# Performance work log

Hardware: AMD Instinct MI355X
Metric: run time of the kernel (lower is better)

The kernel has to match this reference:

```python
import jax, jax.numpy as jnp
import numpy as np

DIM = 1024
N_HEADS = 16


def setup_inputs() -> dict:
    key = jax.random.key(0)
    ks = jax.random.split(key, 9)
    B, S, D = 4, 2048, DIM
    inp = {
        "q": jax.random.normal(ks[0], (B, S, D), dtype=jnp.float32),
        "k": jax.random.normal(ks[1], (B, S, D), dtype=jnp.float32),
        "v": jax.random.normal(ks[2], (B, S, D), dtype=jnp.float32),
        "mask": jnp.ones((B, S), dtype=jnp.float32),
        # nn.Linear params for q, k, v projections (weight: [out,in], bias: [out])
        "wq": jax.random.normal(ks[3], (D, D), dtype=jnp.float32) / np.sqrt(D),
        "bq": jnp.zeros((D,), dtype=jnp.float32),
        "wk": jax.random.normal(ks[4], (D, D), dtype=jnp.float32) / np.sqrt(D),
        "bk": jnp.zeros((D,), dtype=jnp.float32),
        "wv": jax.random.normal(ks[5], (D, D), dtype=jnp.float32) / np.sqrt(D),
        "bv": jnp.zeros((D,), dtype=jnp.float32),
    }
    return inp


def reference(q, k, v, mask, wq, bq, wk, bk, wv, bv):
    B, Sq, D = q.shape
    Skv = k.shape[1]
    H = N_HEADS
    Dh = D // H
    # QKV projections (nn.Linear: x @ W^T + b)
    qp = q @ wq.T + bq
    kp = k @ wk.T + bk
    vp = v @ wv.T + bv
    # split heads: (B, S, H, Dh) -> (B, H, S, Dh)
    qh = qp.reshape(B, Sq, H, Dh).transpose(0, 2, 1, 3)
    kh = kp.reshape(B, Skv, H, Dh).transpose(0, 2, 1, 3)
    vh = vp.reshape(B, Skv, H, Dh).transpose(0, 2, 1, 3)
    # scores: (B, H, Sq, Skv)
    scores = jnp.einsum("bhqd,bhkd->bhqk", qh, kh) / np.sqrt(Dh).astype(np.float32)
    # additive mask (mask is (B, kv_len) -> (B, 1, 1, kv_len))
    scores = scores - 10000.0 * (1.0 - mask[:, None, None, :])
    attn = jax.nn.softmax(scores, axis=-1)
    out = jnp.einsum("bhqk,bhkd->bhqd", attn, vh)
    # merge heads: (B, Sq, D)
    out = out.transpose(0, 2, 1, 3).reshape(B, Sq, D)
    return out
```

## Files before the change

### kernel.cpp

```cpp
#include <hip/hip_runtime.h>
#include <hip/hip_bf16.h>
#include <stdint.h>

typedef __attribute__((ext_vector_type(4))) float f32x4;
typedef __attribute__((ext_vector_type(16))) float f32x16;
typedef __attribute__((ext_vector_type(8))) short bf16x8;

#define AS1 __attribute__((address_space(1)))
#define AS3 __attribute__((address_space(3)))

#if defined(__has_builtin)
#if __has_builtin(__builtin_amdgcn_exp2f)
#define EXPF(x) __builtin_amdgcn_exp2f(x)
#define UNITS 1.4426950408889634f
#endif
#endif
#ifndef EXPF
#define EXPF(x) __expf(x)
#define UNITS 1.0f
#endif

static __device__ __forceinline__ unsigned short f2bf(float f) {
  union { float f; unsigned u; } v; v.f = f;
  unsigned r = v.u + 0x7fffu + ((v.u >> 16) & 1u);
  return (unsigned short)(r >> 16);
}

static __device__ __forceinline__ unsigned pkbf(float lo, float hi) {
  __hip_bfloat162 h2 = __float22bfloat162_rn(make_float2(lo, hi));
  union { __hip_bfloat162 h; unsigned u; } c; c.h = h2; return c.u;
}

__global__ __launch_bounds__(256) void conv_all(
    const float* __restrict__ q, const float* __restrict__ k, const float* __restrict__ v,
    const float* __restrict__ wq, const float* __restrict__ wk, const float* __restrict__ wv,
    unsigned short* __restrict__ Xq, unsigned short* __restrict__ Xk, unsigned short* __restrict__ Xv,
    unsigned short* __restrict__ Wq, unsigned short* __restrict__ Wk, unsigned short* __restrict__ Wv) {
  int bid = blockIdx.x;
  const float* src; unsigned short* dst; int base;
  if (bid < 12288) {
    int t = bid >> 12;
    base = (bid & 4095) * 2048;
    if (t == 0) { src = q; dst = Xq; }
    else if (t == 1) { src = k; dst = Xk; }
    else { src = v; dst = Xv; }
  } else {
    int r = bid - 12288;
    int t = r >> 9;
    base = (r & 511) * 2048;
    if (t == 0) { src = wq; dst = Wq; }
    else if (t == 1) { src = wk; dst = Wk; }
    else { src = wv; dst = Wv; }
  }
  int i = base + threadIdx.x * 8;
  float4 x0 = *(const float4*)(src + i);
  float4 x1 = *(const float4*)(src + i + 4);
  ushort4 o0, o1;
  o0.x = f2bf(x0.x); o0.y = f2bf(x0.y); o0.z = f2bf(x0.z); o0.w = f2bf(x0.w);
  o1.x = f2bf(x1.x); o1.y = f2bf(x1.y); o1.z = f2bf(x1.z); o1.w = f2bf(x1.w);
  *(ushort4*)(dst + i) = o0;
  *(ushort4*)(dst + i + 4) = o1;
}

__global__ __launch_bounds__(256) void proj_gemm3(
    const unsigned short* __restrict__ Xq, const unsigned short* __restrict__ Xk,
    const unsigned short* __restrict__ Xv,
    const unsigned short* __restrict__ Wqp, const unsigned short* __restrict__ Wkp,
    const unsigned short* __restrict__ Wvp,
    const float* __restrict__ bq, const float* __restrict__ bk, const float* __restrict__ bv,
    unsigned short* __restrict__ Qh, unsigned short* __restrict__ Kh,
    unsigned short* __restrict__ Vt) {
  const int K = 1024, S = 2048, H = 16;
  int z = blockIdx.z;
  const unsigned short *A, *W; const float* bias; unsigned short* dst; int transpose_v;
  if (z == 0)      { A = Xq; W = Wqp; bias = bq; dst = Qh; transpose_v = 0; }
  else if (z == 1) { A = Xk; W = Wkp; bias = bk; dst = Kh; transpose_v = 0; }
  else             { A = Xv; W = Wvp; bias = bv; dst = Vt; transpose_v = 1; }

  __shared__ unsigned short As[128 * 32];
  __shared__ unsigned short Bs[128 * 32];
  const int tid = threadIdx.x;
  const int l = tid & 63;
  const int w = tid >> 6;
  const int m0 = blockIdx.x * 128, n0 = blockIdx.y * 128;
  const int wm = w >> 1, wn = w & 1;

  f32x4 acc[4][4] = {};

  const int srow = (l >> 2);
  const int skc = (l & 3) * 8;

  for (int k0 = 0; k0 < K; k0 += 32) {
#pragma unroll
    for (int i = 0; i < 2; ++i) {
      int slot = w * 2 + i;
      int row = slot * 16 + srow;
      const unsigned short* ga = A + (long)(m0 + row) * K + k0 + skc;
      const unsigned short* gb = W + (long)(n0 + row) * K + k0 + skc;
      __builtin_amdgcn_global_load_lds((const AS1 unsigned int*)ga,
                                       (AS3 unsigned int*)(As + slot * 512 + l * 8),
                                       16, 0, 0);
      __builtin_amdgcn_global_load_lds((const AS1 unsigned int*)gb,
                                       (AS3 unsigned int*)(Bs + slot * 512 + l * 8),
                                       16, 0, 0);
    }
    __syncthreads();

    bf16x8 af[4], bfr[4];
    const int kc = (l >> 4) * 8;
#pragma unroll
    for (int mi = 0; mi < 4; ++mi)
      af[mi] = *(const bf16x8*)&As[(wm * 64 + mi * 16 + (l & 15)) * 32 + kc];
#pragma unroll
    for (int ni = 0; ni < 4; ++ni)
      bfr[ni] = *(const bf16x8*)&Bs[(wn * 64 + ni * 16 + (l & 15)) * 32 + kc];
#pragma unroll
    for (int mi = 0; mi < 4; ++mi)
#pragma unroll
      for (int ni = 0; ni < 4; ++ni)
        acc[mi][ni] = __builtin_amdgcn_mfma_f32_16x16x32_bf16(af[mi], bfr[ni], acc[mi][ni], 0, 0, 0);
    __syncthreads();
  }

#pragma unroll
  for (int ni = 0; ni < 4; ++ni) {
    int col = n0 + wn * 64 + ni * 16 + (l & 15);
    float bv_ = bias[col];
    int h = col >> 6, dh = col & 63;
#pragma unroll
    for (int mi = 0; mi < 4; ++mi) {
#pragma unroll
      for (int r = 0; r < 4; ++r) {
        int m = m0 + wm * 64 + mi * 16 + (l >> 4) * 4 + r;
        int b = m >> 11, s = m & 2047;
        unsigned short obf = f2bf(acc[mi][ni][r] + bv_);
        long addr;
        if (!transpose_v)
          addr = ((long)(b * H + h) * S + s) * 64 + dh;
        else
          addr = ((long)(b * H + h) * 64 + dh) * S + s;
        dst[addr] = obf;
      }
    }
  }
}

__device__ __forceinline__ void stage_tile(const unsigned short* __restrict__ kb,
                                           const unsigned short* __restrict__ vb,
                                           char* Kb, char* Vb, int kv0, int tid) {
  int r = tid >> 3;
  int s = (tid & 7) ^ (r & 7);
  const unsigned short* gk = kb + (kv0 + r) * 64 + s * 8;
  const unsigned short* gv = vb + r * 2048 + kv0 + s * 8;
  __builtin_amdgcn_global_load_lds((const AS1 unsigned int*)gk,
                                   (AS3 unsigned int*)(Kb + tid * 16), 16, 0, 0);
  __builtin_amdgcn_global_load_lds((const AS1 unsigned int*)gv,
                                   (AS3 unsigned int*)(Vb + tid * 16), 16, 0, 0);
}

__device__ __forceinline__ void compute_tile(const char* Kb, const char* Vb,
                                             const bf16x8 (&qf)[4],
                                             const float* __restrict__ smask,
                                             int kv0, int hi, int qc,
                                             f32x16 (&acco)[2], float& m_run, float& lrow) {
  const float kSc = 0.125f * UNITS;
  const float THR = 8.0f * UNITS;
  const int kx = qc & 7;

  bf16x8 kf[2][4], vf[2][4];
#pragma unroll
  for (int ks = 0; ks < 2; ++ks)
#pragma unroll
    for (int dc = 0; dc < 4; ++dc)
      kf[ks][dc] = *(const bf16x8*)(Kb + (ks * 32 + qc) * 128 + (((dc * 2 + hi) ^ kx) * 16));
#pragma unroll
  for (int dt = 0; dt < 2; ++dt)
#pragma unroll
    for (int c2 = 0; c2 < 4; ++c2)
      vf[dt][c2] = *(const bf16x8*)(Vb + (dt * 32 + qc) * 128 + (((c2 * 2 + hi) ^ kx) * 16));

  f32x16 st0 = {}, st1 = {};
  __builtin_amdgcn_s_setprio(1);
#pragma unroll
  for (int dc = 0; dc < 4; ++dc) {
    st0 = __builtin_amdgcn_mfma_f32_32x32x16_bf16(kf[0][dc], qf[dc], st0, 0, 0, 0);
    st1 = __builtin_amdgcn_mfma_f32_32x32x16_bf16(kf[1][dc], qf[dc], st1, 0, 0, 0);
  }
  __builtin_amdgcn_s_setprio(0);

  float mf[2][16];
#pragma unroll
  for (int ks = 0; ks < 2; ++ks)
#pragma unroll
    for (int g = 0; g < 4; ++g) {
      float4 t = *(const float4*)&smask[kv0 + ks * 32 + 4 * hi + g * 8];
      mf[ks][g * 4 + 0] = t.x; mf[ks][g * 4 + 1] = t.y;
      mf[ks][g * 4 + 2] = t.z; mf[ks][g * 4 + 3] = t.w;
    }
  float p[2][16];
#pragma unroll
  for (int r = 0; r < 16; ++r) {
    p[0][r] = fmaf(st0[r], kSc, mf[0][r]);
    p[1][r] = fmaf(st1[r], kSc, mf[1][r]);
  }

  float a0 = p[0][0], a1 = p[0][1], a2 = p[0][2], a3 = p[0][3];
#pragma unroll
  for (int r = 4; r < 16; r += 4) {
    a0 = fmaxf(a0, p[0][r]); a1 = fmaxf(a1, p[0][r + 1]);
    a2 = fmaxf(a2, p[0][r + 2]); a3 = fmaxf(a3, p[0][r + 3]);
  }
#pragma unroll
  for (int r = 0; r < 16; r += 4) {
    a0 = fmaxf(a0, p[1][r]); a1 = fmaxf(a1, p[1][r + 1]);
    a2 = fmaxf(a2, p[1][r + 2]); a3 = fmaxf(a3, p[1][r + 3]);
  }
  float pm = fmaxf(fmaxf(a0, a1), fmaxf(a2, a3));
  pm = fmaxf(pm, __shfl_xor(pm, 32));

  if (!__all(pm <= m_run + THR)) {
    float mnew = fmaxf(m_run, pm);
    float scl = EXPF(m_run - mnew);
    lrow *= scl;
#pragma unroll
    for (int dt = 0; dt < 2; ++dt)
#pragma unroll
      for (int r = 0; r < 16; ++r) acco[dt][r] *= scl;
    m_run = mnew;
  }

  float s0 = 0.f, s1 = 0.f, s2 = 0.f, s3 = 0.f;
#pragma unroll
  for (int ks = 0; ks < 2; ++ks)
#pragma unroll
    for (int r = 0; r < 16; r += 4) {
      p[ks][r]     = EXPF(p[ks][r] - m_run);     s0 += p[ks][r];
      p[ks][r + 1] = EXPF(p[ks][r + 1] - m_run); s1 += p[ks][r + 1];
      p[ks][r + 2] = EXPF(p[ks][r + 2] - m_run); s2 += p[ks][r + 2];
      p[ks][r + 3] = EXPF(p[ks][r + 3] - m_run); s3 += p[ks][r + 3];
    }
  float ps = (s0 + s1) + (s2 + s3);
  ps += __shfl_xor(ps, 32);
  lrow += ps;

#pragma unroll
  for (int ks = 0; ks < 2; ++ks) {
    unsigned cp0 = pkbf(p[ks][0], p[ks][1]);
    unsigned cp1 = pkbf(p[ks][2], p[ks][3]);
    unsigned cp2 = pkbf(p[ks][4], p[ks][5]);
    unsigned cp3 = pkbf(p[ks][6], p[ks][7]);
    unsigned cp4 = pkbf(p[ks][8], p[ks][9]);
    unsigned cp5 = pkbf(p[ks][10], p[ks][11]);
    unsigned cp6 = pkbf(p[ks][12], p[ks][13]);
    unsigned cp7 = pkbf(p[ks][14], p[ks][15]);
    asm volatile("v_permlane32_swap_b32 %0, %1" : "+v"(cp0), "+v"(cp2));
    asm volatile("v_permlane32_swap_b32 %0, %1" : "+v"(cp1), "+v"(cp3));
    asm volatile("v_permlane32_swap_b32 %0, %1" : "+v"(cp4), "+v"(cp6));
    asm volatile("v_permlane32_swap_b32 %0, %1" : "+v"(cp5), "+v"(cp7));
    union { unsigned u[4]; bf16x8 v; } B0, B1;
    B0.u[0] = cp0; B0.u[1] = cp1; B0.u[2] = cp2; B0.u[3] = cp3;
    B1.u[0] = cp4; B1.u[1] = cp5; B1.u[2] = cp6; B1.u[3] = cp7;
    __builtin_amdgcn_s_setprio(1);
    acco[0] = __builtin_amdgcn_mfma_f32_32x32x16_bf16(vf[0][ks * 2 + 0], B0.v, acco[0], 0, 0, 0);
    acco[1] = __builtin_amdgcn_mfma_f32_32x32x16_bf16(vf[1][ks * 2 + 0], B0.v, acco[1], 0, 0, 0);
    acco[0] = __builtin_amdgcn_mfma_f32_32x32x16_bf16(vf[0][ks * 2 + 1], B1.v, acco[0], 0, 0, 0);
    acco[1] = __builtin_amdgcn_mfma_f32_32x32x16_bf16(vf[1][ks * 2 + 1], B1.v, acco[1], 0, 0, 0);
    __builtin_amdgcn_s_setprio(0);
  }
}

__global__ __launch_bounds__(512, 2) void attn_kernel(const unsigned short* __restrict__ qh,
                                                      const unsigned short* __restrict__ kh,
                                                      const unsigned short* __restrict__ vt,
                                                      const float* __restrict__ mask,
                                                      float* __restrict__ out) {
  const int S = 2048;
  int bid = blockIdx.x;
  int xcd = bid & 7, jj = bid >> 3;
  int bh = xcd * 8 + (jj & 7);
  int qblk = jj >> 3;
  int b = bh >> 4, h = bh & 15;
  int tid = threadIdx.x, l = tid & 63, w = tid >> 6;
  int hi = l >> 5, qc = l & 31;

  const unsigned short* qb = qh + (long)bh * S * 64;
  const unsigned short* kb = kh + (long)bh * S * 64;
  const unsigned short* vb = vt + (long)bh * 64 * S;

  __shared__ float smask[2048];
  __shared__ __align__(16) char pool[33280];
  for (int i = tid; i < S; i += 512)
    smask[i] = (-10000.0f * UNITS) * (1.0f - mask[b * S + i]);
  __syncthreads();

  const int q0 = qblk * 256 + w * 32;

  bf16x8 qf[4];
#pragma unroll
  for (int dc = 0; dc < 4; ++dc)
    qf[dc] = *(const bf16x8*)&qb[(q0 + qc) * 64 + dc * 16 + 8 * hi];

  f32x16 acco[2] = {};
  float m_run = -1e30f, lrow = 0.0f;

  stage_tile(kb, vb, pool, pool + 8192, 0, tid);
  __syncthreads();

  for (int t = 0; t < 32; ++t) {
    char* cur = pool + (t & 1) * 16384;
    if (t < 31) {
      char* nxt = pool + ((t + 1) & 1) * 16384;
      stage_tile(kb, vb, nxt, nxt + 8192, (t + 1) * 64, tid);
    }
    compute_tile(cur, cur + 8192, qf, smask, t * 64, hi, qc, acco, m_run, lrow);
    __syncthreads();
  }

  float (*olds)[16][65] = (float (*)[16][65])pool;
  float linv = 1.0f / lrow;
#pragma unroll
  for (int pass = 0; pass < 2; ++pass) {
    if ((qc >> 4) == pass) {
#pragma unroll
      for (int dt = 0; dt < 2; ++dt)
#pragma unroll
        for (int r = 0; r < 16; ++r) {
          int d = dt * 32 + (r & 3) + 8 * (r >> 2) + 4 * hi;
          olds[w][qc & 15][d] = acco[dt][r] * linv;
        }
    }
    asm volatile("s_waitcnt lgkmcnt(0)" ::: "memory");
#pragma unroll
    for (int r = 0; r < 16; ++r) {
      float val = olds[w][r][l];
      out[((long)b * 2048 + q0 + pass * 16 + r) * 1024 + h * 64 + l] = val;
    }
    asm volatile("s_waitcnt lgkmcnt(0)" ::: "memory");
  }
}

extern "C" void kernel_launch(void* const* d_in, const int* in_sizes, int n_in,
                              void* d_out, int out_size, void* d_ws, size_t ws_size,
                              hipStream_t stream) {
  const float* q  = (const float*)d_in[0];
  const float* k  = (const float*)d_in[1];
  const float* v  = (const float*)d_in[2];
  const float* mask = (const float*)d_in[3];
  const float* wq = (const float*)d_in[4];
  const float* bq = (const float*)d_in[5];
  const float* wk = (const float*)d_in[6];
  const float* bk = (const float*)d_in[7];
  const float* wv = (const float*)d_in[8];
  const float* bv = (const float*)d_in[9];
  float* out = (float*)d_out;

  char* ws = (char*)d_ws;
  unsigned short* Xq = (unsigned short*)(ws);
  unsigned short* Xk = (unsigned short*)(ws + 16777216L);
  unsigned short* Xv = (unsigned short*)(ws + 33554432L);
  unsigned short* Wq = (unsigned short*)(ws + 50331648L);
  unsigned short* Wk = (unsigned short*)(ws + 52428800L);
  unsigned short* Wv = (unsigned short*)(ws + 54525952L);
  unsigned short* Qh = (unsigned short*)(ws + 56623104L);
  unsigned short* Kh = (unsigned short*)(ws + 73400320L);
  unsigned short* Vt = (unsigned short*)(ws + 90177536L);

  conv_all<<<13824, 256, 0, stream>>>(q, k, v, wq, wk, wv, Xq, Xk, Xv, Wq, Wk, Wv);

  dim3 ggrid(64, 8, 3);
  proj_gemm3<<<ggrid, 256, 0, stream>>>(Xq, Xk, Xv, Wq, Wk, Wv, bq, bk, bv, Qh, Kh, Vt);

  attn_kernel<<<512, 512, 0, stream>>>(Qh, Kh, Vt, mask, out);
}
```

Measured before the change: 377.2 us.

## Double-buffer projection GEMM and shrink attention blocks with direct mask reads

The projection GEMM now double-buffers its LDS tiles, so the next k-slice loads while MFMAs run on the current one, and one barrier per iteration is dropped. The attention kernel goes from 512-thread blocks covering 256 queries to 256-thread blocks covering 128 queries, launching twice as many blocks at up to 4 per CU. It also stops precomputing the mask in shared memory and instead reads the mask from global memory each tile, transforming it with an FMA. This removes the LDS mask staging and the extra barrier, but each block now repeats the K/V loads for fewer queries and makes repeated global mask reads.

```diff
diff --git a/kernel.cpp b/kernel.cpp
--- a/kernel.cpp
+++ b/kernel.cpp
@@ -77,8 +77,8 @@
   else if (z == 1) { A = Xk; W = Wkp; bias = bk; dst = Kh; transpose_v = 0; }
   else             { A = Xv; W = Wvp; bias = bv; dst = Vt; transpose_v = 1; }
 
-  __shared__ unsigned short As[128 * 32];
-  __shared__ unsigned short Bs[128 * 32];
+  __shared__ unsigned short As[2][128 * 32];
+  __shared__ unsigned short Bs[2][128 * 32];
   const int tid = threadIdx.x;
   const int l = tid & 63;
   const int w = tid >> 6;
@@ -90,37 +90,48 @@
   const int srow = (l >> 2);
   const int skc = (l & 3) * 8;
 
+#define STAGE(buf, k0)                                                            \
+  {                                                                               \
+    _Pragma("unroll")                                                             \
+    for (int i = 0; i < 2; ++i) {                                                 \
+      int slot = w * 2 + i;                                                       \
+      int row = slot * 16 + srow;                                                 \
+      const unsigned short* ga = A + (long)(m0 + row) * K + (k0) + skc;           \
+      const unsigned short* gb = W + (long)(n0 + row) * K + (k0) + skc;           \
+      __builtin_amdgcn_global_load_lds((const AS1 unsigned int*)ga,               \
+                                       (AS3 unsigned int*)(As[buf] + slot * 512 + l * 8), \
+                                       16, 0, 0);                                 \
+      __builtin_amdgcn_global_load_lds((const AS1 unsigned int*)gb,               \
+                                       (AS3 unsigned int*)(Bs[buf] + slot * 512 + l * 8), \
+                                       16, 0, 0);                                 \
+    }                                                                             \
+  }
+
+  STAGE(0, 0);
+  __syncthreads();
+
+  int cur = 0;
   for (int k0 = 0; k0 < K; k0 += 32) {
-#pragma unroll
-    for (int i = 0; i < 2; ++i) {
-      int slot = w * 2 + i;
-      int row = slot * 16 + srow;
-      const unsigned short* ga = A + (long)(m0 + row) * K + k0 + skc;
-      const unsigned short* gb = W + (long)(n0 + row) * K + k0 + skc;
-      __builtin_amdgcn_global_load_lds((const AS1 unsigned int*)ga,
-                                       (AS3 unsigned int*)(As + slot * 512 + l * 8),
-                                       16, 0, 0);
-      __builtin_amdgcn_global_load_lds((const AS1 unsigned int*)gb,
-                                       (AS3 unsigned int*)(Bs + slot * 512 + l * 8),
-                                       16, 0, 0);
-    }
-    __syncthreads();
+    if (k0 + 32 < K) STAGE(cur ^ 1, k0 + 32);
 
     bf16x8 af[4], bfr[4];
     const int kc = (l >> 4) * 8;
 #pragma unroll
     for (int mi = 0; mi < 4; ++mi)
-      af[mi] = *(const bf16x8*)&As[(wm * 64 + mi * 16 + (l & 15)) * 32 + kc];
+      af[mi] = *(const bf16x8*)&As[cur][(wm * 64 + mi * 16 + (l & 15)) * 32 + kc];
 #pragma unroll
     for (int ni = 0; ni < 4; ++ni)
-      bfr[ni] = *(const bf16x8*)&Bs[(wn * 64 + ni * 16 + (l & 15)) * 32 + kc];
+      bfr[ni] = *(const bf16x8*)&Bs[cur][(wn * 64 + ni * 16 + (l & 15)) * 32 + kc];
 #pragma unroll
     for (int mi = 0; mi < 4; ++mi)
 #pragma unroll
       for (int ni = 0; ni < 4; ++ni)
         acc[mi][ni] = __builtin_amdgcn_mfma_f32_16x16x32_bf16(af[mi], bfr[ni], acc[mi][ni], 0, 0, 0);
+
     __syncthreads();
-  }
+    cur ^= 1;
+  }
+#undef STAGE
 
 #pragma unroll
   for (int ni = 0; ni < 4; ++ni) {
@@ -148,23 +159,28 @@
 __device__ __forceinline__ void stage_tile(const unsigned short* __restrict__ kb,
                                            const unsigned short* __restrict__ vb,
                                            char* Kb, char* Vb, int kv0, int tid) {
-  int r = tid >> 3;
-  int s = (tid & 7) ^ (r & 7);
-  const unsigned short* gk = kb + (kv0 + r) * 64 + s * 8;
-  const unsigned short* gv = vb + r * 2048 + kv0 + s * 8;
-  __builtin_amdgcn_global_load_lds((const AS1 unsigned int*)gk,
-                                   (AS3 unsigned int*)(Kb + tid * 16), 16, 0, 0);
-  __builtin_amdgcn_global_load_lds((const AS1 unsigned int*)gv,
-                                   (AS3 unsigned int*)(Vb + tid * 16), 16, 0, 0);
+#pragma unroll
+  for (int j = 0; j < 2; ++j) {
+    int c = tid + j * 256;
+    int r = c >> 3;
+    int s = (c & 7) ^ (r & 7);
+    const unsigned short* gk = kb + (kv0 + r) * 64 + s * 8;
+    const unsigned short* gv = vb + r * 2048 + kv0 + s * 8;
+    __builtin_amdgcn_global_load_lds((const AS1 unsigned int*)gk,
+                                     (AS3 unsigned int*)(Kb + c * 16), 16, 0, 0);
+    __builtin_amdgcn_global_load_lds((const AS1 unsigned int*)gv,
+                                     (AS3 unsigned int*)(Vb + c * 16), 16, 0, 0);
+  }
 }
 
 __device__ __forceinline__ void compute_tile(const char* Kb, const char* Vb,
                                              const bf16x8 (&qf)[4],
-                                             const float* __restrict__ smask,
+                                             const float* __restrict__ mask_b,
                                              int kv0, int hi, int qc,
                                              f32x16 (&acco)[2], float& m_run, float& lrow) {
   const float kSc = 0.125f * UNITS;
   const float THR = 8.0f * UNITS;
+  const float MC = 10000.0f * UNITS;
   const int kx = qc & 7;
 
   bf16x8 kf[2][4], vf[2][4];
@@ -193,9 +209,9 @@
   for (int ks = 0; ks < 2; ++ks)
 #pragma unroll
     for (int g = 0; g < 4; ++g) {
-      float4 t = *(const float4*)&smask[kv0 + ks * 32 + 4 * hi + g * 8];
-      mf[ks][g * 4 + 0] = t.x; mf[ks][g * 4 + 1] = t.y;
-      mf[ks][g * 4 + 2] = t.z; mf[ks][g * 4 + 3] = t.w;
+      float4 t = *(const float4*)&mask_b[kv0 + ks * 32 + 4 * hi + g * 8];
+      mf[ks][g * 4 + 0] = fmaf(t.x, MC, -MC); mf[ks][g * 4 + 1] = fmaf(t.y, MC, -MC);
+      mf[ks][g * 4 + 2] = fmaf(t.z, MC, -MC); mf[ks][g * 4 + 3] = fmaf(t.w, MC, -MC);
     }
   float p[2][16];
 #pragma unroll
@@ -269,7 +285,7 @@
   }
 }
 
-__global__ __launch_bounds__(512, 2) void attn_kernel(const unsigned short* __restrict__ qh,
+__global__ __launch_bounds__(256, 4) void attn_kernel(const unsigned short* __restrict__ qh,
                                                       const unsigned short* __restrict__ kh,
                                                       const unsigned short* __restrict__ vt,
                                                       const float* __restrict__ mask,
@@ -286,14 +302,11 @@
   const unsigned short* qb = qh + (long)bh * S * 64;
   const unsigned short* kb = kh + (long)bh * S * 64;
   const unsigned short* vb = vt + (long)bh * 64 * S;
-
-  __shared__ float smask[2048];
-  __shared__ __align__(16) char pool[33280];
-  for (int i = tid; i < S; i += 512)
-    smask[i] = (-10000.0f * UNITS) * (1.0f - mask[b * S + i]);
-  __syncthreads();
-
-  const int q0 = qblk * 256 + w * 32;
+  const float* mask_b = mask + (long)b * S;
+
+  __shared__ __align__(16) char pool[32768];
+
+  const int q0 = qblk * 128 + w * 32;
 
   bf16x8 qf[4];
 #pragma unroll
@@ -312,7 +325,7 @@
       char* nxt = pool + ((t + 1) & 1) * 16384;
       stage_tile(kb, vb, nxt, nxt + 8192, (t + 1) * 64, tid);
     }
-    compute_tile(cur, cur + 8192, qf, smask, t * 64, hi, qc, acco, m_run, lrow);
+    compute_tile(cur, cur + 8192, qf, mask_b, t * 64, hi, qc, acco, m_run, lrow);
     __syncthreads();
   }
 
@@ -370,5 +383,5 @@
   dim3 ggrid(64, 8, 3);
   proj_gemm3<<<ggrid, 256, 0, stream>>>(Xq, Xk, Xv, Wq, Wk, Wv, bq, bk, bv, Qh, Kh, Vt);
 
-  attn_kernel<<<512, 512, 0, stream>>>(Qh, Kh, Vt, mask, out);
-}
+  attn_kernel<<<1024, 256, 0, stream>>>(Qh, Kh, Vt, mask, out);
+}
```

Result: slower. 758.2 us (+101.0%).
